# Optimization experiments

Hardware: AMD Instinct MI355X
Metric: run time of the kernel (lower is better)

## Reference

```python
import jax, jax.numpy as jnp
import numpy as np

DIM = 768
HEADS = 12
B, N = 1, 4096


def setup_inputs() -> dict:
    key = jax.random.key(0)
    k1, k2, k3 = jax.random.split(key, 3)
    x = jax.random.normal(k1, (B, N, DIM), dtype=jnp.float32)
    W_qkv = jax.random.normal(k2, (DIM, 3 * DIM), dtype=jnp.float32) * (DIM ** -0.5)
    W_out = jax.random.normal(k3, (DIM, DIM), dtype=jnp.float32) * (DIM ** -0.5)
    b_out = jnp.zeros((DIM,), dtype=jnp.float32)
    return {"x": x, "W_qkv": W_qkv, "W_out": W_out, "b_out": b_out}


def reference(x, W_qkv, W_out, b_out):
    b, n, dim = x.shape
    h = HEADS
    d = dim // h
    qkv = x @ W_qkv  # [b, n, 3*dim]
    q, k, v = jnp.split(qkv, 3, axis=-1)
    # 'b n (h d) -> b h n d'
    def to_heads(a):
        return a.reshape(b, n, h, d).transpose(0, 2, 1, 3)
    q, k, v = to_heads(q), to_heads(k), to_heads(v)
    # NOTE: original module computes self.scale but never applies it -> unscaled dots
    dots = jnp.einsum('bhid,bhjd->bhij', q, k)
    attn = jax.nn.softmax(dots, axis=-1)
    out = jnp.einsum('bhij,bhjd->bhid', attn, v)
    out = out.transpose(0, 2, 1, 3).reshape(b, n, dim)  # 'b h n d -> b n (h d)'
    return out @ W_out + b_out
```

## Files before the change

kernel.cpp:

```cpp
#include <hip/hip_runtime.h>

typedef unsigned short ushort_t;
typedef unsigned int uint_t;
typedef __bf16 bf16x8 __attribute__((ext_vector_type(8)));
typedef __bf16 bf16x4 __attribute__((ext_vector_type(4)));
typedef float f32x4 __attribute__((ext_vector_type(4)));
typedef ushort_t u16x4 __attribute__((ext_vector_type(4)));

#define NSEQ 4096
#define DIMM 768
#define NQKV 2304
#define HEADS 12
#define LOG2E 1.4426950408889634f

#if __has_builtin(__builtin_amdgcn_exp2f)
#define EXP2(x) __builtin_amdgcn_exp2f(x)
#else
#define EXP2(x) exp2f(x)
#endif


__device__ __forceinline__ ushort_t f2bf(float f) {
    uint_t u = __float_as_uint(f);
    u = u + 0x7fffu + ((u >> 16) & 1u);
    return (ushort_t)(u >> 16);
}
__device__ __forceinline__ f32x4 zero4() {
    f32x4 v = {0.f, 0.f, 0.f, 0.f};
    return v;
}

__device__ __forceinline__ void pack_w_tile(const float* __restrict__ src,
                                            ushort_t* __restrict__ dst,
                                            int K, int N, int bk, int bn, int t,
                                            ushort_t* Ls) {
    const int tr = t >> 4, tc = t & 15;
#pragma unroll
    for (int i = 0; i < 4; ++i) {
        int r = tr + 16 * i;
        float4 v = *(const float4*)(&src[(size_t)(bk + r) * N + bn + tc * 4]);
        const float* vv = (const float*)&v;
#pragma unroll
        for (int j = 0; j < 4; ++j) Ls[(tc * 4 + j) * 72 + r] = f2bf(vv[j]);
    }
    __syncthreads();
    const int KB = K >> 3;
    const int n = t >> 2;
    const int ks = t & 3;
    const int gn = bn + n;
    size_t base = ((size_t)(gn >> 4) * KB + ((bk + ks * 16) >> 3)) * 128 + (gn & 15) * 8;
    *(uint4*)(&dst[base])       = *(const uint4*)(&Ls[n * 72 + ks * 16]);
    *(uint4*)(&dst[base + 128]) = *(const uint4*)(&Ls[n * 72 + ks * 16 + 8]);
}

#define CVT_BLOCKS   3072
#define PW1_BLOCKS   (12 * 36)
#define PW2_BLOCKS   (12 * 12)

__global__ __launch_bounds__(256) void prep_kernel(
    const float* __restrict__ X, const float* __restrict__ Wqkv, const float* __restrict__ Wout,
    ushort_t* __restrict__ Ap, ushort_t* __restrict__ Wqp, ushort_t* __restrict__ Wop)
{
    __shared__ ushort_t Ls[64 * 72];
    const int b = blockIdx.x;
    const int t = threadIdx.x;
    if (b < CVT_BLOCKS) {
        int i = b * 256 + t;
        int row = i / (DIMM / 4);
        int k0 = (i - row * (DIMM / 4)) * 4;
        float4 v = *(const float4*)(&X[(size_t)row * DIMM + k0]);
        u16x4 p = { f2bf(v.x), f2bf(v.y), f2bf(v.z), f2bf(v.w) };
        size_t idx = ((size_t)(row >> 4) * (DIMM / 8) + (k0 >> 3)) * 128 + (row & 15) * 8 + (k0 & 7);
        *(u16x4*)(&Ap[idx]) = p;
    } else if (b < CVT_BLOCKS + PW1_BLOCKS) {
        int j = b - CVT_BLOCKS;
        pack_w_tile(Wqkv, Wqp, DIMM, NQKV, (j % 12) * 64, (j / 12) * 64, t, Ls);
    } else {
        int j = b - CVT_BLOCKS - PW1_BLOCKS;
        pack_w_tile(Wout, Wop, DIMM, DIMM, (j % 12) * 64, (j / 12) * 64, t, Ls);
    }
}

#define QKV_LOAD(af, bfv, kt) do {                                                            \
    _Pragma("unroll")                                                                         \
    for (int mi = 0; mi < 4; ++mi)                                                            \
        af[mi] = *(const bf16x8*)(&Ap[((size_t)(amb + mi) * KB + (kt) * 4 + g) * 128 + m16 * 8]); \
    _Pragma("unroll")                                                                         \
    for (int nj = 0; nj < 4; ++nj)                                                            \
        bfv[nj] = *(const bf16x8*)(&Bp[((size_t)(bnb + nj) * KB + (kt) * 4 + g) * 128 + m16 * 8]); \
} while (0)

__global__ __launch_bounds__(256) void qkv_gemm_kernel(
    const ushort_t* __restrict__ Ap, const ushort_t* __restrict__ Bp,
    ushort_t* __restrict__ Qp, ushort_t* __restrict__ Kp, ushort_t* __restrict__ Vp)
{
    const int t = threadIdx.x;
    const int lane = t & 63;
    const int w = t >> 6;
    const int m16 = lane & 15;
    const int g = lane >> 4;
    const int wrow = (w >> 1) * 64;
    const int wcol = (w & 1) * 64;
    const int bm = blockIdx.y * 128;
    const int bn = blockIdx.x * 128;
    const int amb = (bm + wrow) >> 4;
    const int bnb = (bn + wcol) >> 4;
    const int KB = DIMM / 8;
    const int which = bn / DIMM;

    f32x4 acc[4][4];
#pragma unroll
    for (int i = 0; i < 4; ++i)
#pragma unroll
        for (int j = 0; j < 4; ++j) acc[i][j] = zero4();

    bf16x8 af0[4], bf0[4], af1[4], bf1[4];
    QKV_LOAD(af0, bf0, 0);

    if (which < 2) {
        for (int kt = 0; kt < 24; kt += 2) {
            QKV_LOAD(af1, bf1, kt + 1);
#pragma unroll
            for (int mi = 0; mi < 4; ++mi)
#pragma unroll
                for (int nj = 0; nj < 4; ++nj)
                    acc[mi][nj] = __builtin_amdgcn_mfma_f32_16x16x32_bf16(bf0[nj], af0[mi], acc[mi][nj], 0, 0, 0);
            if (kt + 2 < 24) QKV_LOAD(af0, bf0, kt + 2);
#pragma unroll
            for (int mi = 0; mi < 4; ++mi)
#pragma unroll
                for (int nj = 0; nj < 4; ++nj)
                    acc[mi][nj] = __builtin_amdgcn_mfma_f32_16x16x32_bf16(bf1[nj], af1[mi], acc[mi][nj], 0, 0, 0);
        }
        ushort_t* dst = (which == 0) ? Qp : Kp;
        const float scale = (which == 0) ? LOG2E : 1.0f;
        const int cb = bn - which * DIMM + wcol;
        const int h = cb >> 6;
        const int ghi = g >> 1, glo = g & 1;
#pragma unroll
        for (int mi = 0; mi < 4; ++mi) {
            int sblk = amb + mi;
#pragma unroll
            for (int nj = 0; nj < 4; ++nj) {
                size_t idx = (((size_t)h * 256 + sblk) * 8 + nj * 2 + ghi) * 128 + m16 * 8 + glo * 4;
                u16x4 pk = { f2bf(acc[mi][nj][0] * scale), f2bf(acc[mi][nj][1] * scale),
                             f2bf(acc[mi][nj][2] * scale), f2bf(acc[mi][nj][3] * scale) };
                *(u16x4*)(&dst[idx]) = pk;
            }
        }
    } else {
        for (int kt = 0; kt < 24; kt += 2) {
            QKV_LOAD(af1, bf1, kt + 1);
#pragma unroll
            for (int mi = 0; mi < 4; ++mi)
#pragma unroll
                for (int nj = 0; nj < 4; ++nj)
                    acc[mi][nj] = __builtin_amdgcn_mfma_f32_16x16x32_bf16(af0[mi], bf0[nj], acc[mi][nj], 0, 0, 0);
            if (kt + 2 < 24) QKV_LOAD(af0, bf0, kt + 2);
#pragma unroll
            for (int mi = 0; mi < 4; ++mi)
#pragma unroll
                for (int nj = 0; nj < 4; ++nj)
                    acc[mi][nj] = __builtin_amdgcn_mfma_f32_16x16x32_bf16(af1[mi], bf1[nj], acc[mi][nj], 0, 0, 0);
        }
        const int cb = bn - 2 * DIMM + wcol;
        const int h = cb >> 6;
        const int ghi = g >> 1, glo = g & 1;
        const int kb8 = (bm + wrow) >> 3;
#pragma unroll
        for (int mi = 0; mi < 4; ++mi) {
#pragma unroll
            for (int nj = 0; nj < 4; ++nj) {
                size_t idx = (((size_t)h * 512 + kb8 + mi * 2 + ghi) * 4 + nj) * 128 + m16 * 8 + glo * 4;
                u16x4 pk = { f2bf(acc[mi][nj][0]), f2bf(acc[mi][nj][1]),
                             f2bf(acc[mi][nj][2]), f2bf(acc[mi][nj][3]) };
                *(u16x4*)(&Vp[idx]) = pk;
            }
        }
    }
}

__global__ __launch_bounds__(256, 4) void attn_kernel(
    const ushort_t* __restrict__ Qp, const ushort_t* __restrict__ Kp,
    const ushort_t* __restrict__ Vp, float* __restrict__ Opart, float* __restrict__ Lpart,
    int niter)
{
    __shared__ ushort_t Ps[4][32 * 72];
    const int t = threadIdx.x;
    const int lane = t & 63;
    const int w = t >> 6;
    const int m16 = lane & 15;
    const int g = lane >> 4;
    const int h = blockIdx.y;
    const int half = blockIdx.z;
    const int qb = blockIdx.x * 128 + w * 32;
    const int qblk0 = qb >> 4;
    const int kblk0 = half * niter * 4;
    const int vblk0 = half * niter * 8;

    bf16x8 qf[2][2];
#pragma unroll
    for (int mi = 0; mi < 2; ++mi)
#pragma unroll
        for (int kd = 0; kd < 2; ++kd)
            qf[mi][kd] = *(const bf16x8*)(&Qp[(((size_t)h * 256 + qblk0 + mi) * 8 + kd * 4 + g) * 128 + m16 * 8]);

    const ushort_t* kpA = Kp + ((size_t)h * 256 + kblk0) * 1024 + g * 128 + m16 * 8;
    const ushort_t* kpB = kpA + 2048;
    const ushort_t* vpA = Vp + ((size_t)h * 512 + vblk0) * 512 + g * 512 + m16 * 8;
    const ushort_t* vpB = vpA + 2048;

    f32x4 oacc[2][4];
#pragma unroll
    for (int mi = 0; mi < 2; ++mi)
#pragma unroll
        for (int dj = 0; dj < 4; ++dj) oacc[mi][dj] = zero4();
    f32x4 lacc[2] = {zero4(), zero4()};

#pragma unroll 4
    for (int kt = 0; kt < niter; ++kt) {
        bf16x8 kf[4][2];
        kf[0][0] = *(const bf16x8*)(kpA);
        kf[0][1] = *(const bf16x8*)(kpA + 512);
        kf[1][0] = *(const bf16x8*)(kpA + 1024);
        kf[1][1] = *(const bf16x8*)(kpA + 1536);
        kf[2][0] = *(const bf16x8*)(kpB);
        kf[2][1] = *(const bf16x8*)(kpB + 512);
        kf[3][0] = *(const bf16x8*)(kpB + 1024);
        kf[3][1] = *(const bf16x8*)(kpB + 1536);
        bf16x8 vf[4][2];
#pragma unroll
        for (int dj = 0; dj < 4; ++dj) {
            vf[dj][0] = *(const bf16x8*)(vpA + dj * 128);
            vf[dj][1] = *(const bf16x8*)(vpB + dj * 128);
        }
        kpA += 4096; kpB += 4096; vpA += 4096; vpB += 4096;

#pragma unroll
        for (int nj = 0; nj < 4; ++nj) {
#pragma unroll
            for (int mi = 0; mi < 2; ++mi) {
                f32x4 st = zero4();
#pragma unroll
                for (int kd = 0; kd < 2; ++kd)
                    st = __builtin_amdgcn_mfma_f32_16x16x32_bf16(kf[nj][kd], qf[mi][kd], st, 0, 0, 0);
                f32x4 p;
#pragma unroll
                for (int r = 0; r < 4; ++r) p[r] = EXP2(st[r]);
                lacc[mi] += p;
                bf16x4 pk = { (__bf16)p[0], (__bf16)p[1], (__bf16)p[2], (__bf16)p[3] };
                *(bf16x4*)(&Ps[w][(mi * 16 + m16) * 72 + nj * 16 + g * 4]) = pk;
            }
        }
        bf16x8 pf[2][2];
#pragma unroll
        for (int mi = 0; mi < 2; ++mi)
#pragma unroll
            for (int kc = 0; kc < 2; ++kc)
                pf[mi][kc] = *(const bf16x8*)(&Ps[w][(mi * 16 + m16) * 72 + kc * 32 + g * 8]);
#pragma unroll
        for (int mi = 0; mi < 2; ++mi)
#pragma unroll
            for (int dj = 0; dj < 4; ++dj)
#pragma unroll
                for (int kc = 0; kc < 2; ++kc)
                    oacc[mi][dj] = __builtin_amdgcn_mfma_f32_16x16x32_bf16(pf[mi][kc], vf[dj][kc], oacc[mi][dj], 0, 0, 0);
    }

    float* Oph = Opart + (size_t)half * NSEQ * DIMM;
    float* Lph = Lpart + (size_t)half * HEADS * NSEQ + (size_t)h * NSEQ;
#pragma unroll
    for (int mi = 0; mi < 2; ++mi) {
        float l = (lacc[mi][0] + lacc[mi][1]) + (lacc[mi][2] + lacc[mi][3]);
        l += __shfl_xor(l, 16);
        l += __shfl_xor(l, 32);
        if (g == 0) Lph[qb + mi * 16 + m16] = l;
    }
#pragma unroll
    for (int mi = 0; mi < 2; ++mi) {
#pragma unroll
        for (int r = 0; r < 4; ++r) {
            int row = qb + mi * 16 + g * 4 + r;
#pragma unroll
            for (int dj = 0; dj < 4; ++dj)
                Oph[(size_t)row * DIMM + h * 64 + dj * 16 + m16] = oacc[mi][dj][r];
        }
    }
}

__global__ __launch_bounds__(256) void merge_kernel(
    const float* __restrict__ Opart, const float* __restrict__ Lpart,
    ushort_t* __restrict__ Xap, int nsplit)
{
    int i = blockIdx.x * 256 + threadIdx.x;
    int row = i / (DIMM / 4);
    int col0 = (i - row * (DIMM / 4)) * 4;
    int h = col0 >> 6;
    float l = 0.f;
    f32x4 o = zero4();
    for (int s = 0; s < nsplit; ++s) {
        l += Lpart[(size_t)s * HEADS * NSEQ + (size_t)h * NSEQ + row];
        f32x4 ov = *(const f32x4*)(&Opart[(size_t)s * NSEQ * DIMM + (size_t)row * DIMM + col0]);
        o += ov;
    }
    float inv = 1.0f / l;
    u16x4 p = { f2bf(o[0] * inv), f2bf(o[1] * inv), f2bf(o[2] * inv), f2bf(o[3] * inv) };
    size_t idx = ((size_t)(row >> 4) * (DIMM / 8) + (col0 >> 3)) * 128 + (row & 15) * 8 + (col0 & 7);
    *(u16x4*)(&Xap[idx]) = p;
}

__global__ __launch_bounds__(64, 4) void out_gemm_kernel(
    const ushort_t* __restrict__ Ap, const ushort_t* __restrict__ Bp,
    const float* __restrict__ bias, float* __restrict__ out)
{
    const int lane = threadIdx.x & 63;
    const int m16 = lane & 15;
    const int g = lane >> 4;
    const int bm = blockIdx.y * 32;
    const int bn = blockIdx.x * 64;
    const int amb = bm >> 4;
    const int bnb = bn >> 4;
    const int KB = DIMM / 8;

    f32x4 acc[2][4];
#pragma unroll
    for (int i = 0; i < 2; ++i)
#pragma unroll
        for (int j = 0; j < 4; ++j) acc[i][j] = zero4();

#pragma unroll 2
    for (int kt = 0; kt < 24; ++kt) {
        bf16x8 af[2], bfv[4];
#pragma unroll
        for (int mi = 0; mi < 2; ++mi)
            af[mi] = *(const bf16x8*)(&Ap[((size_t)(amb + mi) * KB + kt * 4 + g) * 128 + m16 * 8]);
#pragma unroll
        for (int nj = 0; nj < 4; ++nj)
            bfv[nj] = *(const bf16x8*)(&Bp[((size_t)(bnb + nj) * KB + kt * 4 + g) * 128 + m16 * 8]);
#pragma unroll
        for (int mi = 0; mi < 2; ++mi)
#pragma unroll
            for (int nj = 0; nj < 4; ++nj)
                acc[mi][nj] = __builtin_amdgcn_mfma_f32_16x16x32_bf16(af[mi], bfv[nj], acc[mi][nj], 0, 0, 0);
    }
#pragma unroll
    for (int mi = 0; mi < 2; ++mi) {
#pragma unroll
        for (int nj = 0; nj < 4; ++nj) {
            int col = bn + nj * 16 + m16;
            float bv = bias[col];
#pragma unroll
            for (int r = 0; r < 4; ++r) {
                int row = bm + mi * 16 + g * 4 + r;
                out[(size_t)row * DIMM + col] = acc[mi][nj][r] + bv;
            }
        }
    }
}

extern "C" void kernel_launch(void* const* d_in, const int* in_sizes, int n_in,
                              void* d_out, int out_size, void* d_ws, size_t ws_size,
                              hipStream_t stream) {
    (void)in_sizes; (void)n_in; (void)out_size;
    const float* X    = (const float*)d_in[0];
    const float* Wqkv = (const float*)d_in[1];
    const float* Wout = (const float*)d_in[2];
    const float* bout = (const float*)d_in[3];
    float* out = (float*)d_out;

    const size_t TSZ = (size_t)NSEQ * DIMM;
    const size_t fixed = TSZ * 2 * 5 + (size_t)NQKV * DIMM * 2 + (size_t)DIMM * DIMM * 2;
    const size_t per_split = TSZ * 4 + (size_t)HEADS * NSEQ * 4;
    const int nsplit = (ws_size >= fixed + 4 * per_split) ? 4 : 2;

    unsigned char* p = (unsigned char*)d_ws;
    ushort_t* Ap  = (ushort_t*)p; p += TSZ * 2;
    ushort_t* Wqp = (ushort_t*)p; p += (size_t)NQKV * DIMM * 2;
    ushort_t* Wop = (ushort_t*)p; p += (size_t)DIMM * DIMM * 2;
    ushort_t* Qp  = (ushort_t*)p; p += TSZ * 2;
    ushort_t* Kp  = (ushort_t*)p; p += TSZ * 2;
    ushort_t* Vp  = (ushort_t*)p; p += TSZ * 2;
    ushort_t* Xap = (ushort_t*)p; p += TSZ * 2;
    float* Opart  = (float*)p;    p += (size_t)nsplit * TSZ * 4;
    float* Lpart  = (float*)p;

    const int niter = (NSEQ / 64) / nsplit;

    prep_kernel<<<CVT_BLOCKS + PW1_BLOCKS + PW2_BLOCKS, 256, 0, stream>>>(X, Wqkv, Wout, Ap, Wqp, Wop);
    qkv_gemm_kernel<<<dim3(NQKV / 128, NSEQ / 128), 256, 0, stream>>>(Ap, Wqp, Qp, Kp, Vp);
    attn_kernel<<<dim3(NSEQ / 128, HEADS, nsplit), 256, 0, stream>>>(Qp, Kp, Vp, Opart, Lpart, niter);
    merge_kernel<<<TSZ / 4 / 256, 256, 0, stream>>>(Opart, Lpart, Xap, nsplit);
    out_gemm_kernel<<<dim3(DIMM / 64, NSEQ / 32), 64, 0, stream>>>(Xap, Wop, bout, out);
}
```

Before: 201.4 us.

## Software-pipeline K loads in attention loop and compute row sums via MFMA

```diff
diff --git a/kernel.cpp b/kernel.cpp
--- a/kernel.cpp
+++ b/kernel.cpp
@@ -180,12 +180,46 @@
     }
 }
 
+#define ATTN_LOADK(dst, ptr) do {                          \
+    dst[0][0] = *(const bf16x8*)(ptr);                     \
+    dst[0][1] = *(const bf16x8*)((ptr) + 512);             \
+    dst[1][0] = *(const bf16x8*)((ptr) + 1024);            \
+    dst[1][1] = *(const bf16x8*)((ptr) + 1536);            \
+} while (0)
+
+#define ATTN_LOADV(dst, ptr) do {                          \
+    dst[0] = *(const bf16x8*)(ptr);                        \
+    dst[1] = *(const bf16x8*)((ptr) + 128);                \
+    dst[2] = *(const bf16x8*)((ptr) + 256);                \
+    dst[3] = *(const bf16x8*)((ptr) + 384);                \
+} while (0)
+
+#define ATTN_COMPUTE(KF, VF) do {                                                             \
+    _Pragma("unroll")                                                                         \
+    for (int mi = 0; mi < 2; ++mi) {                                                          \
+        _Pragma("unroll")                                                                     \
+        for (int nj = 0; nj < 2; ++nj) {                                                      \
+            f32x4 st = zero4();                                                               \
+            st = __builtin_amdgcn_mfma_f32_16x16x32_bf16(KF[nj][0], qf[mi][0], st, 0, 0, 0);  \
+            st = __builtin_amdgcn_mfma_f32_16x16x32_bf16(KF[nj][1], qf[mi][1], st, 0, 0, 0);  \
+            bf16x4 pk = { (__bf16)EXP2(st[0]), (__bf16)EXP2(st[1]),                           \
+                          (__bf16)EXP2(st[2]), (__bf16)EXP2(st[3]) };                         \
+            *(bf16x4*)(&Ps[w][(mi * 16 + m16) * 40 + nj * 16 + g * 4]) = pk;                  \
+        }                                                                                     \
+        bf16x8 pf = *(const bf16x8*)(&Ps[w][(mi * 16 + m16) * 40 + g * 8]);                   \
+        lfrag[mi] = __builtin_amdgcn_mfma_f32_16x16x32_bf16(pf, onesf, lfrag[mi], 0, 0, 0);   \
+        _Pragma("unroll")                                                                     \
+        for (int dj = 0; dj < 4; ++dj)                                                        \
+            oacc[mi][dj] = __builtin_amdgcn_mfma_f32_16x16x32_bf16(pf, VF[dj], oacc[mi][dj], 0, 0, 0); \
+    }                                                                                         \
+} while (0)
+
 __global__ __launch_bounds__(256, 4) void attn_kernel(
     const ushort_t* __restrict__ Qp, const ushort_t* __restrict__ Kp,
     const ushort_t* __restrict__ Vp, float* __restrict__ Opart, float* __restrict__ Lpart,
     int niter)
 {
-    __shared__ ushort_t Ps[4][32 * 72];
+    __shared__ ushort_t Ps[4][32 * 40];
     const int t = threadIdx.x;
     const int lane = t & 63;
     const int w = t >> 6;
@@ -205,76 +239,43 @@
         for (int kd = 0; kd < 2; ++kd)
             qf[mi][kd] = *(const bf16x8*)(&Qp[(((size_t)h * 256 + qblk0 + mi) * 8 + kd * 4 + g) * 128 + m16 * 8]);
 
-    const ushort_t* kpA = Kp + ((size_t)h * 256 + kblk0) * 1024 + g * 128 + m16 * 8;
-    const ushort_t* kpB = kpA + 2048;
-    const ushort_t* vpA = Vp + ((size_t)h * 512 + vblk0) * 512 + g * 512 + m16 * 8;
-    const ushort_t* vpB = vpA + 2048;
+    const ushort_t* kp = Kp + ((size_t)h * 256 + kblk0) * 1024 + g * 128 + m16 * 8;
+    const ushort_t* vp = Vp + ((size_t)h * 512 + vblk0) * 512 + g * 512 + m16 * 8;
+
+    bf16x8 onesf;
+#pragma unroll
+    for (int i = 0; i < 8; ++i) onesf[i] = (__bf16)1.0f;
 
     f32x4 oacc[2][4];
 #pragma unroll
     for (int mi = 0; mi < 2; ++mi)
 #pragma unroll
         for (int dj = 0; dj < 4; ++dj) oacc[mi][dj] = zero4();
-    f32x4 lacc[2] = {zero4(), zero4()};
-
-#pragma unroll 4
-    for (int kt = 0; kt < niter; ++kt) {
-        bf16x8 kf[4][2];
-        kf[0][0] = *(const bf16x8*)(kpA);
-        kf[0][1] = *(const bf16x8*)(kpA + 512);
-        kf[1][0] = *(const bf16x8*)(kpA + 1024);
-        kf[1][1] = *(const bf16x8*)(kpA + 1536);
-        kf[2][0] = *(const bf16x8*)(kpB);
-        kf[2][1] = *(const bf16x8*)(kpB + 512);
-        kf[3][0] = *(const bf16x8*)(kpB + 1024);
-        kf[3][1] = *(const bf16x8*)(kpB + 1536);
-        bf16x8 vf[4][2];
-#pragma unroll
-        for (int dj = 0; dj < 4; ++dj) {
-            vf[dj][0] = *(const bf16x8*)(vpA + dj * 128);
-            vf[dj][1] = *(const bf16x8*)(vpB + dj * 128);
-        }
-        kpA += 4096; kpB += 4096; vpA += 4096; vpB += 4096;
-
-#pragma unroll
-        for (int nj = 0; nj < 4; ++nj) {
-#pragma unroll
-            for (int mi = 0; mi < 2; ++mi) {
-                f32x4 st = zero4();
-#pragma unroll
-                for (int kd = 0; kd < 2; ++kd)
-                    st = __builtin_amdgcn_mfma_f32_16x16x32_bf16(kf[nj][kd], qf[mi][kd], st, 0, 0, 0);
-                f32x4 p;
-#pragma unroll
-                for (int r = 0; r < 4; ++r) p[r] = EXP2(st[r]);
-                lacc[mi] += p;
-                bf16x4 pk = { (__bf16)p[0], (__bf16)p[1], (__bf16)p[2], (__bf16)p[3] };
-                *(bf16x4*)(&Ps[w][(mi * 16 + m16) * 72 + nj * 16 + g * 4]) = pk;
-            }
-        }
-        bf16x8 pf[2][2];
-#pragma unroll
-        for (int mi = 0; mi < 2; ++mi)
-#pragma unroll
-            for (int kc = 0; kc < 2; ++kc)
-                pf[mi][kc] = *(const bf16x8*)(&Ps[w][(mi * 16 + m16) * 72 + kc * 32 + g * 8]);
-#pragma unroll
-        for (int mi = 0; mi < 2; ++mi)
-#pragma unroll
-            for (int dj = 0; dj < 4; ++dj)
-#pragma unroll
-                for (int kc = 0; kc < 2; ++kc)
-                    oacc[mi][dj] = __builtin_amdgcn_mfma_f32_16x16x32_bf16(pf[mi][kc], vf[dj][kc], oacc[mi][dj], 0, 0, 0);
+    f32x4 lfrag[2] = {zero4(), zero4()};
+
+    bf16x8 ka[2][2], kb[2][2];
+    ATTN_LOADK(ka, kp); kp += 2048;
+
+    const int nsteps = niter * 2;
+    for (int s = 0; s < nsteps; s += 2) {
+        bf16x8 va[4];
+        ATTN_LOADV(va, vp); vp += 2048;
+        ATTN_LOADK(kb, kp); kp += 2048;
+        ATTN_COMPUTE(ka, va);
+        bf16x8 vb[4];
+        ATTN_LOADV(vb, vp); vp += 2048;
+        ATTN_LOADK(ka, kp); kp += 2048;
+        ATTN_COMPUTE(kb, vb);
     }
 
     float* Oph = Opart + (size_t)half * NSEQ * DIMM;
     float* Lph = Lpart + (size_t)half * HEADS * NSEQ + (size_t)h * NSEQ;
-#pragma unroll
-    for (int mi = 0; mi < 2; ++mi) {
-        float l = (lacc[mi][0] + lacc[mi][1]) + (lacc[mi][2] + lacc[mi][3]);
-        l += __shfl_xor(l, 16);
-        l += __shfl_xor(l, 32);
-        if (g == 0) Lph[qb + mi * 16 + m16] = l;
+    if (m16 == 0) {
+#pragma unroll
+        for (int mi = 0; mi < 2; ++mi)
+#pragma unroll
+            for (int r = 0; r < 4; ++r)
+                Lph[qb + mi * 16 + g * 4 + r] = lfrag[mi][r];
     }
 #pragma unroll
     for (int mi = 0; mi < 2; ++mi) {
```

New measurement: 204.3 us. Within noise of the previous version (+1.4%).
